# Kernel tuning notes

Hardware: AMD Instinct MI355X
Metric: run time of the kernel (lower is better)

Reference implementation:

```python
import jax, jax.numpy as jnp
import numpy as np


def _norm_group(pts, ref):
    # pts: [B,T,N,2], ref: [B,T,1,2]. Subtract reference point, divide both coords
    # by max(width,height) of the relative bbox (per frame), guarding scale==0.
    rel = pts - ref
    w = rel[..., 0].max(axis=-1) - rel[..., 0].min(axis=-1)
    h = rel[..., 1].max(axis=-1) - rel[..., 1].min(axis=-1)
    s = jnp.maximum(w, h)
    s = jnp.where(s == 0, jnp.ones_like(s), s)
    return rel / s[..., None, None]


def _prepare_input(x):
    B, T, _ = x.shape
    pts = x.reshape(B, T, 133, 2)
    left = _norm_group(pts[:, :, 91:112], pts[:, :, 9:10]).reshape(B, T, 42)
    right = _norm_group(pts[:, :, 112:133], pts[:, :, 10:11]).reshape(B, T, 42)
    center = pts[:, :, 0:1]
    left_arm = _norm_group(pts[:, :, (5, 7, 9), :], center).reshape(B, T, 6)
    right_arm = _norm_group(pts[:, :, (6, 8, 10), :], center).reshape(B, T, 6)
    return right, right_arm, left, left_arm


def _lstm(x, wih, whh, bih, bhh):
    # x: [B,T,F]; PyTorch gate order i,f,g,o. Returns all hidden states [B,T,H].
    B = x.shape[0]
    H = whh.shape[1]
    pre = jnp.einsum('btf,gf->btg', x, wih) + bih  # [B,T,4H]
    pre = pre.transpose(1, 0, 2)  # time-major for scan
    h0 = jnp.zeros((B, H), x.dtype)
    c0 = jnp.zeros((B, H), x.dtype)

    def step(carry, xt):
        h, c = carry
        g = xt + h @ whh.T + bhh
        i, f, gg, o = jnp.split(g, 4, axis=-1)
        i = jax.nn.sigmoid(i)
        f = jax.nn.sigmoid(f)
        gg = jnp.tanh(gg)
        o = jax.nn.sigmoid(o)
        c = f * c + i * gg
        h = o * jnp.tanh(c)
        return (h, c), h

    _, hs = jax.lax.scan(step, (h0, c0), pre)
    return hs.transpose(1, 0, 2)


def setup_inputs() -> dict:
    key = jax.random.key(0)
    ks = jax.random.split(key, 24)
    B, T = 128, 512
    NUM_CLASSES = 250
    HID = 2 * 64 + 2 * 32  # 192
    s = 0.1

    def p(k, shape):
        return jax.random.normal(k, shape, dtype=jnp.float32) * s

    inp = {'x': jax.random.normal(ks[0], (B, T, 266), dtype=jnp.float32)}
    # right hand LSTM: 42 -> 64
    inp['wih_rh'] = p(ks[1], (256, 42)); inp['whh_rh'] = p(ks[2], (256, 64))
    inp['bih_rh'] = p(ks[3], (256,));   inp['bhh_rh'] = p(ks[4], (256,))
    # right arm LSTM: 6 -> 32
    inp['wih_ra'] = p(ks[5], (128, 6));  inp['whh_ra'] = p(ks[6], (128, 32))
    inp['bih_ra'] = p(ks[7], (128,));   inp['bhh_ra'] = p(ks[8], (128,))
    # left hand LSTM: 42 -> 64
    inp['wih_lh'] = p(ks[9], (256, 42)); inp['whh_lh'] = p(ks[10], (256, 64))
    inp['bih_lh'] = p(ks[11], (256,));  inp['bhh_lh'] = p(ks[12], (256,))
    # left arm LSTM: 6 -> 32
    inp['wih_la'] = p(ks[13], (128, 6)); inp['whh_la'] = p(ks[14], (128, 32))
    inp['bih_la'] = p(ks[15], (128,));  inp['bhh_la'] = p(ks[16], (128,))
    # attention (Linear(192,1,bias=False)) and fc
    inp['att_w'] = p(ks[17], (1, HID))
    inp['fc_w'] = p(ks[18], (NUM_CLASSES, HID))
    inp['fc_b'] = p(ks[19], (NUM_CLASSES,))
    return inp


def reference(x, wih_rh, whh_rh, bih_rh, bhh_rh,
              wih_ra, whh_ra, bih_ra, bhh_ra,
              wih_lh, whh_lh, bih_lh, bhh_lh,
              wih_la, whh_la, bih_la, bhh_la,
              att_w, fc_w, fc_b):
    rh, ra, lh, la = _prepare_input(x)
    rh_out = _lstm(rh, wih_rh, whh_rh, bih_rh, bhh_rh)
    ra_out = _lstm(ra, wih_ra, whh_ra, bih_ra, bhh_ra)
    lh_out = _lstm(lh, wih_lh, whh_lh, bih_lh, bhh_lh)
    la_out = _lstm(la, wih_la, whh_la, bih_la, bhh_la)
    combined = jnp.concatenate([rh_out, ra_out, lh_out, la_out], axis=2)  # [B,T,192]
    scores = jnp.einsum('bth,oh->bto', combined, att_w)  # [B,T,1]
    weights = jax.nn.softmax(scores, axis=1)
    context = jnp.sum(weights * combined, axis=1)  # [B,192]
    out = context @ fc_w.T + fc_b  # [B,num_classes]
    return out, weights
```

## Files before the change

kernel.cpp:

```cpp
#include <hip/hip_runtime.h>
#include <math.h>

#define BATCH 128
#define TLEN 512
#define XF 266
#define HID 192
#define NC 250

typedef __attribute__((ext_vector_type(8))) short short8;
typedef __attribute__((ext_vector_type(4))) float float4v;

#define NL2E  -1.4426950408889634f
#define NL2E2 -2.8853900817779268f

__device__ __forceinline__ unsigned short f2bf(float f) {
  unsigned u = __float_as_uint(f);
  u += 0x7FFF + ((u >> 16) & 1);
  return (unsigned short)(u >> 16);
}
__device__ __forceinline__ float bf2f(unsigned short s) {
  return __uint_as_float(((unsigned)s) << 16);
}

__device__ __forceinline__ float exp2i(float x) {
#if __has_builtin(__builtin_amdgcn_exp2f)
  return __builtin_amdgcn_exp2f(x);
#else
  float r;
  asm("v_exp_f32 %0, %1" : "=v"(r) : "v"(x));
  return r;
#endif
}

__device__ __forceinline__ void lds_barrier() {
  asm volatile("s_waitcnt lgkmcnt(0)\n\ts_barrier" ::: "memory");
}


__device__ __forceinline__ void norm_hand(const float* __restrict__ xp,
                                          unsigned short* __restrict__ fp,
                                          int p0, int refp, int hs) {
  float rx = xp[2 * refp], ry = xp[2 * refp + 1];
  float px[21], py[21];
  float minx = 1e30f, maxx = -1e30f, miny = 1e30f, maxy = -1e30f;
#pragma unroll
  for (int i = 0; i < 21; ++i) {
    float ax = xp[2 * (p0 + i)] - rx;
    float ay = xp[2 * (p0 + i) + 1] - ry;
    px[i] = ax; py[i] = ay;
    minx = fminf(minx, ax); maxx = fmaxf(maxx, ax);
    miny = fminf(miny, ay); maxy = fmaxf(maxy, ay);
  }
  float s = fmaxf(maxx - minx, maxy - miny);
  if (s == 0.f) s = 1.f;
  float inv = 1.f / s;
#pragma unroll
  for (int i = 0; i < 21; ++i) {
    fp[2 * i] = f2bf(px[i] * inv);
    fp[2 * i + 1] = f2bf(py[i] * inv);
  }
  for (int i = 42; i < hs; ++i) fp[i] = 0;
}

__device__ __forceinline__ void norm_arm(const float* __restrict__ xp,
                                         unsigned short* __restrict__ fp,
                                         int a, int b, int c) {
  float rx = xp[0], ry = xp[1];
  float x0 = xp[2 * a] - rx, y0 = xp[2 * a + 1] - ry;
  float x1 = xp[2 * b] - rx, y1 = xp[2 * b + 1] - ry;
  float x2 = xp[2 * c] - rx, y2 = xp[2 * c + 1] - ry;
  float w = fmaxf(fmaxf(x0, x1), x2) - fminf(fminf(x0, x1), x2);
  float h = fmaxf(fmaxf(y0, y1), y2) - fminf(fminf(y0, y1), y2);
  float s = fmaxf(w, h);
  if (s == 0.f) s = 1.f;
  float inv = 1.f / s;
  fp[0] = f2bf(x0 * inv); fp[1] = f2bf(y0 * inv);
  fp[2] = f2bf(x1 * inv); fp[3] = f2bf(y1 * inv);
  fp[4] = f2bf(x2 * inv); fp[5] = f2bf(y2 * inv);
  fp[6] = 0; fp[7] = 0;
}

__global__ __launch_bounds__(256) void prep_kernel(
    const float* __restrict__ x,
    unsigned short* __restrict__ fHR, unsigned short* __restrict__ fHL,
    unsigned short* __restrict__ fAR, unsigned short* __restrict__ fAL,
    int mode) {
  int idx = blockIdx.x * 256 + threadIdx.x;
  if (idx >= BATCH * TLEN) return;
  int b = idx >> 9, t = idx & 511;
  const float* xp = x + (size_t)idx * XF;
  size_t hoff, aoff;
  int hs;
  if (mode) {
    hs = 64;
    int vh = b & 7;
    int rowh = (vh >> 1) * 4 + (vh & 1);
    hoff = (((size_t)(b >> 3) * TLEN + t) * 16 + rowh) * 64;
    int va = b & 15;
    int rowa = (va >> 3) * 16 + ((va & 7) >> 1) * 4 + (va & 1);
    aoff = (((size_t)(b >> 4) * TLEN + t) * 32 + rowa) * 8;
  } else {
    hs = 48;
    hoff = (((size_t)(b >> 4) * TLEN + t) * 16 + (b & 15)) * 48;
    aoff = (((size_t)(b >> 5) * TLEN + t) * 32 + (b & 31)) * 8;
  }
  norm_hand(xp, fHR + hoff, 112, 10, hs);
  norm_hand(xp, fHL + hoff, 91, 9, hs);
  norm_arm (xp, fAR + aoff, 6, 8, 10);
  norm_arm (xp, fAL + aoff, 5, 7, 9);
}


__global__ __launch_bounds__(256) void pack_kernel(
    int mode,
    const float* __restrict__ wi_rh, const float* __restrict__ wh_rh,
    const float* __restrict__ wi_ra, const float* __restrict__ wh_ra,
    const float* __restrict__ wi_lh, const float* __restrict__ wh_lh,
    const float* __restrict__ wi_la, const float* __restrict__ wh_la,
    unsigned short* __restrict__ btA_r, unsigned short* __restrict__ btA_l,
    unsigned short* __restrict__ btH_r, unsigned short* __restrict__ btH_l,
    unsigned short* __restrict__ btArm_r, unsigned short* __restrict__ btArm_l) {
  int blk = blockIdx.x, tid = threadIdx.x;
  if (blk < 2) {
    const float* wi = blk ? wi_lh : wi_rh;
    const float* wh = blk ? wh_lh : wh_rh;
    unsigned short* dst = blk ? btA_l : btA_r;
    if (mode) {
      for (int i = tid; i < 256 * 64; i += 256) {
        int g = i >> 6, k = i & 63;
        float s = ((g >> 6) == 2) ? NL2E2 : NL2E;
        dst[i] = f2bf(k < 42 ? wi[g * 42 + k] * s : 0.f);
      }
    } else {
      for (int i = tid; i < 256 * 128; i += 256) {
        int g = i >> 7, k = i & 127;
        float s = ((g >> 6) == 2) ? NL2E2 : NL2E;
        float v = (k < 42) ? wi[g * 42 + k] : (k < 64 ? 0.f : wh[g * 64 + (k - 64)]);
        dst[i] = f2bf(v * s);
      }
    }
  } else if (blk < 4) {
    if (mode) {
      const float* wh = (blk == 3) ? wh_lh : wh_rh;
      unsigned short* dst = (blk == 3) ? btH_l : btH_r;
      for (int i = tid; i < 256 * 64; i += 256) {
        int g = i >> 6;
        float s = ((g >> 6) == 2) ? NL2E2 : NL2E;
        dst[i] = f2bf(wh[i] * s);
      }
    }
  } else {
    const float* wi = (blk == 5) ? wi_la : wi_ra;
    const float* wh = (blk == 5) ? wh_la : wh_ra;
    unsigned short* dst = (blk == 5) ? btArm_l : btArm_r;
    for (int i = tid; i < 128 * 64; i += 256) {
      int g = i >> 6, k = i & 63;
      float s = ((g >> 5) == 2) ? NL2E2 : NL2E;
      float v = (k < 6) ? wi[g * 6 + k] : (k < 32 ? 0.f : wh[g * 32 + (k - 32)]);
      dst[i] = f2bf(v * s);
    }
  }
}


__global__ __launch_bounds__(256, 1) void pregemm_kernel(
    const unsigned short* __restrict__ f64R, const unsigned short* __restrict__ f64L,
    const unsigned short* __restrict__ btiR, const unsigned short* __restrict__ btiL,
    const float* __restrict__ biR, const float* __restrict__ bhR,
    const float* __restrict__ biL, const float* __restrict__ bhL,
    unsigned short* __restrict__ preR, unsigned short* __restrict__ preL) {
  int bx = blockIdx.x;
  int lr = bx >> 8, tile = (bx >> 4) & 15, tc = bx & 15;
  const unsigned short* f64 = lr ? f64L : f64R;
  const unsigned short* bti = lr ? btiL : btiR;
  const float* bi = lr ? biL : biR;
  const float* bh = lr ? bhL : bhR;
  unsigned short* pre = lr ? preL : preR;
  int tid = threadIdx.x, lane = tid & 63;
  int q = tid >> 6, n = lane & 15, quad = lane >> 4;
  float sq = (q == 2) ? NL2E2 : NL2E;

  short8 Vb[4][2];
  float bias[4];
#pragma unroll
  for (int jg = 0; jg < 4; ++jg) {
    int g = q * 64 + jg * 16 + n;
    bias[jg] = (bi[g] + bh[g]) * sq;
#pragma unroll
    for (int c = 0; c < 2; ++c)
      Vb[jg][c] = *(const short8*)(bti + (size_t)g * 64 + c * 32 + quad * 8);
  }

  for (int i = 0; i < 32; ++i) {
    int t = tc * 32 + i;
    const unsigned short* ap = f64 + ((size_t)(tile * 512 + t) * 16 + n) * 64 + quad * 8;
    short8 Va0 = *(const short8*)ap;
    short8 Va1 = *(const short8*)(ap + 32);
    unsigned short* pb = pre + (size_t)(tile * 512 + t) * 2048 + n * 32 + quad * 8 + q * 2;
#pragma unroll
    for (int jg = 0; jg < 4; ++jg) {
      float4v acc = {bias[jg], bias[jg], bias[jg], bias[jg]};
      acc = __builtin_amdgcn_mfma_f32_16x16x32_bf16(Va0, Vb[jg][0], acc, 0, 0, 0);
      acc = __builtin_amdgcn_mfma_f32_16x16x32_bf16(Va1, Vb[jg][1], acc, 0, 0, 0);
      unsigned w = (unsigned)f2bf(acc[0]) | ((unsigned)f2bf(acc[1]) << 16);
      *(unsigned*)(pb + (size_t)jg * 512) = w;
    }
  }
}


template <int H, int CH, int STR, int MB, int SCH, int HOFF, bool HOIST, int RV>
__device__ __forceinline__ void lstm_core(
    unsigned short* __restrict__ Ab0, unsigned short* __restrict__ Ab1,
    const unsigned short* __restrict__ Bt,
    const float* __restrict__ bi, const float* __restrict__ bh,
    const unsigned short* __restrict__ featp,
    const unsigned short* __restrict__ prep_,
    unsigned short* __restrict__ combbase,
    int b0, int mrow0, int j0) {
  constexpr int K = CH * 32;
  constexpr int XSH = MB * SCH * 8;
  constexpr int JQ = H / 4;
  constexpr int VR = (RV == 4) ? MB : MB / 2;
  int tid = threadIdx.x;
  int lane = tid & 63, n = lane & 15, quad = lane >> 4;

  short8 Vb[4][CH];
  float bias[4];
#pragma unroll
  for (int q = 0; q < 4; ++q) {
    int g = q * H + j0 + n;
    if (!HOIST) bias[q] = (bi[g] + bh[g]) * ((q == 2) ? NL2E2 : NL2E);
#pragma unroll
    for (int c = 0; c < CH; ++c)
      Vb[q][c] = *(const short8*)(Bt + (size_t)g * K + c * 32 + quad * 8);
  }

  for (int i = tid; i < MB * STR; i += 256) { Ab0[i] = 0; Ab1[i] = 0; }
  __syncthreads();

  bool st = false;
  unsigned short *xd0 = nullptr, *xd1 = nullptr;
  const unsigned short* fp = nullptr;
  short8 xE, xO;
  if (!HOIST) {
    st = tid < MB * SCH;
    int sm = tid / SCH, sc8 = tid % SCH;
    xd0 = Ab0 + sm * STR + sc8 * 8;
    xd1 = Ab1 + sm * STR + sc8 * 8;
    fp = featp + tid * 8;
    if (st) {
      *(short8*)xd0 = *(const short8*)fp;
      xO = *(const short8*)(fp + XSH);
      xE = *(const short8*)(fp + 2 * (size_t)XSH);
    }
    fp += 3 * (size_t)XSH;
  }

  const unsigned short* ppE = nullptr;
  const unsigned short* ppO = nullptr;
  short8 pE, pO;
  if (HOIST) {
    const unsigned short* pp0 = prep_ + (size_t)j0 * 32 + n * 32 + quad * 8;
    pE = *(const short8*)pp0;
    pO = *(const short8*)(pp0 + 2048);
    ppE = pp0 + 2 * (size_t)2048;
    ppO = pp0 + 3 * (size_t)2048;
  }

  float4v cc = {0.f, 0.f, 0.f, 0.f};
  __syncthreads();

  const unsigned short* ard0 = Ab0 + (mrow0 + n) * STR;
  const unsigned short* ard1 = Ab1 + (mrow0 + n) * STR;
  unsigned short* hw0 = Ab0 + (mrow0 + quad * 4) * STR + HOFF + j0 + n;
  unsigned short* hw1 = Ab1 + (mrow0 + quad * 4) * STR + HOFF + j0 + n;

  int vi = tid / JQ, fjq = tid % JQ;
  bool fon = tid < VR * JQ;
  int fm = (RV == 4) ? vi
                     : ((vi >> 3) * 16 + ((vi & 7) >> 1) * 4 + (vi & 1));
  const unsigned short* fl0 = Ab0 + fm * STR + HOFF + fjq * 4;
  const unsigned short* fl1 = Ab1 + fm * STR + HOFF + fjq * 4;
  unsigned short* cfp = combbase + ((size_t)(b0 + vi) * TLEN) * HID + fjq * 4;

#define ACT_AND_WRITE(hw)                                                     \
  _Pragma("unroll")                                                           \
  for (int r = 0; r < RV; ++r) {                                              \
    float Ei = exp2i(acc[0][r]);                                              \
    float Ef = exp2i(acc[1][r]);                                              \
    float Eg = exp2i(acc[2][r]);                                              \
    float Eo = exp2i(acc[3][r]);                                              \
    float gf = __builtin_amdgcn_rcpf(1.f + Ef);                               \
    float ig = (1.f - Eg) * __builtin_amdgcn_rcpf((1.f + Ei) * (1.f + Eg));   \
    float cv = fmaf(gf, cc[r], ig);                                           \
    cc[r] = cv;                                                               \
    float Ec = exp2i(cv * NL2E2);                                             \
    float hv = (1.f - Ec) * __builtin_amdgcn_rcpf((1.f + Eo) * (1.f + Ec));   \
    (hw)[r * STR] = f2bf(hv);                                                 \
  }

  for (int tt = 0; tt < TLEN; tt += 2) {
    {
      const int t = tt;
      if (fon && t > 0) {
        *(uint2*)cfp = *(const uint2*)fl0;
        cfp += HID;
      }
      short8 Va[CH];
#pragma unroll
      for (int c = 0; c < CH; ++c)
        Va[c] = *(const short8*)(ard0 + c * 32 + quad * 8);

      float4v acc[4];
      if (HOIST) {
#pragma unroll
        for (int q = 0; q < 4; ++q) {
          acc[q][0] = bf2f((unsigned short)pE[q * 2]);
          acc[q][1] = bf2f((unsigned short)pE[q * 2 + 1]);
          acc[q][2] = 0.f; acc[q][3] = 0.f;
        }
        if (t + 2 < TLEN) pE = *(const short8*)ppE;
        ppE += 2 * (size_t)2048;
      } else {
#pragma unroll
        for (int q = 0; q < 4; ++q)
          acc[q] = (float4v){bias[q], bias[q], bias[q], bias[q]};
      }
#pragma unroll
      for (int q = 0; q < 4; ++q)
#pragma unroll
        for (int c = 0; c < CH; ++c)
          acc[q] = __builtin_amdgcn_mfma_f32_16x16x32_bf16(Va[c], Vb[q][c], acc[q], 0, 0, 0);

      if (!HOIST) {
        if (st) {
          *(short8*)xd1 = xO;
          if (t + 3 < TLEN) xO = *(const short8*)fp;
        }
        fp += XSH;
      }

      ACT_AND_WRITE(hw1)
      lds_barrier();
    }
    {
      const int t = tt + 1;
      if (fon) {
        *(uint2*)cfp = *(const uint2*)fl1;
        cfp += HID;
      }
      short8 Va[CH];
#pragma unroll
      for (int c = 0; c < CH; ++c)
        Va[c] = *(const short8*)(ard1 + c * 32 + quad * 8);

      float4v acc[4];
      if (HOIST) {
#pragma unroll
        for (int q = 0; q < 4; ++q) {
          acc[q][0] = bf2f((unsigned short)pO[q * 2]);
          acc[q][1] = bf2f((unsigned short)pO[q * 2 + 1]);
          acc[q][2] = 0.f; acc[q][3] = 0.f;
        }
        if (t + 2 < TLEN) pO = *(const short8*)ppO;
        ppO += 2 * (size_t)2048;
      } else {
#pragma unroll
        for (int q = 0; q < 4; ++q)
          acc[q] = (float4v){bias[q], bias[q], bias[q], bias[q]};
      }
#pragma unroll
      for (int q = 0; q < 4; ++q)
#pragma unroll
        for (int c = 0; c < CH; ++c)
          acc[q] = __builtin_amdgcn_mfma_f32_16x16x32_bf16(Va[c], Vb[q][c], acc[q], 0, 0, 0);

      if (!HOIST) {
        if (st) {
          if (t + 1 < TLEN) *(short8*)xd0 = xE;
          if (t + 3 < TLEN) xE = *(const short8*)fp;
        }
        fp += XSH;
      }

      ACT_AND_WRITE(hw0)
      lds_barrier();
    }
  }

  if (fon) *(uint2*)cfp = *(const uint2*)fl0;
#undef ACT_AND_WRITE
}

__global__ __launch_bounds__(256, 1) void lstm_hoist(
    const unsigned short* __restrict__ fAR, const unsigned short* __restrict__ fAL,
    const unsigned short* __restrict__ btH_r, const unsigned short* __restrict__ btH_l,
    const unsigned short* __restrict__ btArm_r, const unsigned short* __restrict__ btArm_l,
    const unsigned short* __restrict__ preR, const unsigned short* __restrict__ preL,
    const float* __restrict__ b1i, const float* __restrict__ b1h,
    const float* __restrict__ b3i, const float* __restrict__ b3h,
    unsigned short* __restrict__ combined) {
  __shared__ __align__(16) unsigned short A0[2304];
  __shared__ __align__(16) unsigned short A1[2304];
  int blk = blockIdx.x;
  int wave = threadIdx.x >> 6;
  if (blk < 32) {
    int lr = blk >> 4, tl = blk & 15;
    lstm_core<64, 2, 72, 16, 0, 0, true, 2>(
        A0, A1, lr ? btH_l : btH_r, nullptr, nullptr, nullptr,
        (lr ? preL : preR) + (size_t)tl * 512 * 2048,
        combined + (lr ? 96 : 0), tl * 8, 0, wave * 16);
  } else {
    int a = blk - 32;
    int la = a >> 3, tl = a & 7;
    lstm_core<32, 2, 72, 32, 1, 32, false, 2>(
        A0, A1, la ? btArm_l : btArm_r, la ? b3i : b1i, la ? b3h : b1h,
        (la ? fAL : fAR) + (size_t)tl * 512 * 256, nullptr,
        combined + (la ? 160 : 64), tl * 16, (wave >> 1) * 16, (wave & 1) * 16);
  }
}

__global__ __launch_bounds__(256, 1) void lstm_fb(
    const unsigned short* __restrict__ fHR, const unsigned short* __restrict__ fHL,
    const unsigned short* __restrict__ fAR, const unsigned short* __restrict__ fAL,
    const unsigned short* __restrict__ btA_r, const unsigned short* __restrict__ btA_l,
    const unsigned short* __restrict__ btArm_r, const unsigned short* __restrict__ btArm_l,
    const float* __restrict__ b0i, const float* __restrict__ b0h,
    const float* __restrict__ b1i, const float* __restrict__ b1h,
    const float* __restrict__ b2i, const float* __restrict__ b2h,
    const float* __restrict__ b3i, const float* __restrict__ b3h,
    unsigned short* __restrict__ combined) {
  __shared__ __align__(16) unsigned short A0[2304];
  __shared__ __align__(16) unsigned short A1[2304];
  int blk = blockIdx.x;
  int wave = threadIdx.x >> 6;
  if (blk < 16) {
    int lr = blk >> 3, tl = blk & 7;
    lstm_core<64, 4, 136, 16, 6, 64, false, 4>(
        A0, A1, lr ? btA_l : btA_r, lr ? b2i : b0i, lr ? b2h : b0h,
        (lr ? fHL : fHR) + (size_t)tl * 512 * 768, nullptr,
        combined + (lr ? 96 : 0), tl * 16, 0, wave * 16);
  } else {
    int a = blk - 16;
    int la = a >> 2, tl = a & 3;
    lstm_core<32, 2, 72, 32, 1, 32, false, 4>(
        A0, A1, la ? btArm_l : btArm_r, la ? b3i : b1i, la ? b3h : b1h,
        (la ? fAL : fAR) + (size_t)tl * 512 * 256, nullptr,
        combined + (la ? 160 : 64), tl * 32, (wave >> 1) * 16, (wave & 1) * 16);
  }
}


__global__ __launch_bounds__(512) void attn_kernel(const unsigned short* __restrict__ combined,
                                                   const float* __restrict__ att_w,
                                                   const float* __restrict__ fc_w,
                                                   const float* __restrict__ fc_b,
                                                   float* __restrict__ dout) {
  __shared__ float sc[TLEN];
  __shared__ float aw[HID];
  __shared__ float pctx[8][HID];
  __shared__ float ctx[HID];
  __shared__ float red[8];
  int b = blockIdx.x, tid = threadIdx.x;
  int lane = tid & 63, wave = tid >> 6;
  const unsigned short* cb = combined + (size_t)b * TLEN * HID;
  if (tid < HID) aw[tid] = att_w[tid];
  __syncthreads();
  float a0 = aw[lane], a1 = aw[lane + 64], a2 = aw[lane + 128];

  int t0 = wave * 64;
  for (int t = t0; t < t0 + 64; t += 2) {
    const unsigned short* r0 = cb + (size_t)t * HID;
    const unsigned short* r1 = r0 + HID;
    float p0 = a0 * bf2f(r0[lane]) + a1 * bf2f(r0[lane + 64]) + a2 * bf2f(r0[lane + 128]);
    float p1 = a0 * bf2f(r1[lane]) + a1 * bf2f(r1[lane + 64]) + a2 * bf2f(r1[lane + 128]);
#pragma unroll
    for (int o = 32; o; o >>= 1) {
      p0 += __shfl_xor(p0, o, 64);
      p1 += __shfl_xor(p1, o, 64);
    }
    if (lane == 0) { sc[t] = p0; sc[t + 1] = p1; }
  }
  __syncthreads();

  float e = sc[tid];
  float lmax = e;
#pragma unroll
  for (int o = 32; o; o >>= 1) lmax = fmaxf(lmax, __shfl_xor(lmax, o, 64));
  if (lane == 0) red[wave] = lmax;
  __syncthreads();
  float m = red[0];
#pragma unroll
  for (int w = 1; w < 8; ++w) m = fmaxf(m, red[w]);
  __syncthreads();
  float ex = __expf(e - m);
  float ls = ex;
#pragma unroll
  for (int o = 32; o; o >>= 1) ls += __shfl_xor(ls, o, 64);
  if (lane == 0) red[wave] = ls;
  __syncthreads();
  float S = red[0];
#pragma unroll
  for (int w = 1; w < 8; ++w) S += red[w];
  float wgt = ex / S;
  sc[tid] = wgt;
  dout[BATCH * NC + b * TLEN + tid] = wgt;
  __syncthreads();

#pragma unroll
  for (int p = 0; p < 3; ++p) {
    int h = p * 64 + lane;
    float c0 = 0.f, c1 = 0.f, c2 = 0.f, c3 = 0.f;
    for (int t = t0; t < t0 + 64; t += 4) {
      c0 += sc[t] * bf2f(cb[(size_t)t * HID + h]);
      c1 += sc[t + 1] * bf2f(cb[(size_t)(t + 1) * HID + h]);
      c2 += sc[t + 2] * bf2f(cb[(size_t)(t + 2) * HID + h]);
      c3 += sc[t + 3] * bf2f(cb[(size_t)(t + 3) * HID + h]);
    }
    pctx[wave][h] = (c0 + c1) + (c2 + c3);
  }
  __syncthreads();
  if (tid < HID) {
    float s = pctx[0][tid];
#pragma unroll
    for (int w = 1; w < 8; ++w) s += pctx[w][tid];
    ctx[tid] = s;
  }
  __syncthreads();

  if (tid < NC) {
    const float* wr = fc_w + (size_t)tid * HID;
    float s0 = fc_b[tid], s1 = 0.f, s2 = 0.f, s3 = 0.f;
#pragma unroll
    for (int h = 0; h < HID; h += 4) {
      s0 += ctx[h] * wr[h];
      s1 += ctx[h + 1] * wr[h + 1];
      s2 += ctx[h + 2] * wr[h + 2];
      s3 += ctx[h + 3] * wr[h + 3];
    }
    dout[b * NC + tid] = (s0 + s1) + (s2 + s3);
  }
}


extern "C" void kernel_launch(void* const* d_in, const int* in_sizes, int n_in,
                              void* d_out, int out_size, void* d_ws, size_t ws_size,
                              hipStream_t stream) {
  const float* x = (const float*)d_in[0];
  const float* wih_rh = (const float*)d_in[1];
  const float* whh_rh = (const float*)d_in[2];
  const float* bih_rh = (const float*)d_in[3];
  const float* bhh_rh = (const float*)d_in[4];
  const float* wih_ra = (const float*)d_in[5];
  const float* whh_ra = (const float*)d_in[6];
  const float* bih_ra = (const float*)d_in[7];
  const float* bhh_ra = (const float*)d_in[8];
  const float* wih_lh = (const float*)d_in[9];
  const float* whh_lh = (const float*)d_in[10];
  const float* bih_lh = (const float*)d_in[11];
  const float* bhh_lh = (const float*)d_in[12];
  const float* wih_la = (const float*)d_in[13];
  const float* whh_la = (const float*)d_in[14];
  const float* bih_la = (const float*)d_in[15];
  const float* bhh_la = (const float*)d_in[16];
  const float* att_w = (const float*)d_in[17];
  const float* fc_w = (const float*)d_in[18];
  const float* fc_b = (const float*)d_in[19];

  const size_t SZ_COMB   = (size_t)BATCH * TLEN * HID * 2;
  const size_t SZ_FARM_H = (size_t)8 * TLEN * 32 * 8 * 2;
  const size_t SZ_FARM_F = (size_t)4 * TLEN * 32 * 8 * 2;
  const size_t SZ_F64    = (size_t)16 * TLEN * 16 * 64 * 2;
  const size_t SZ_F48    = (size_t)8 * TLEN * 16 * 48 * 2;
  const size_t SZ_PRE    = (size_t)16 * TLEN * 2048 * 2;
  const size_t NEED_FULL = SZ_COMB + 2 * SZ_FARM_H + 2 * SZ_F64 + 2 * SZ_PRE +
                           2 * 32768 + 2 * 32768 + 2 * 16384;
  bool hoist = ws_size >= NEED_FULL;

  char* p = (char*)d_ws;
  unsigned short* combined = (unsigned short*)p; p += SZ_COMB;
  unsigned short *fAR, *fAL;
  unsigned short *fHR, *fHL, *preR = nullptr, *preL = nullptr;
  unsigned short *btA_r, *btA_l, *btH_r = nullptr, *btH_l = nullptr, *btArm_r, *btArm_l;
  if (hoist) {
    fAR = (unsigned short*)p; p += SZ_FARM_H;
    fAL = (unsigned short*)p; p += SZ_FARM_H;
    fHR = (unsigned short*)p; p += SZ_F64;
    fHL = (unsigned short*)p; p += SZ_F64;
    preR = (unsigned short*)p; p += SZ_PRE;
    preL = (unsigned short*)p; p += SZ_PRE;
    btA_r = (unsigned short*)p; p += 32768;
    btA_l = (unsigned short*)p; p += 32768;
    btH_r = (unsigned short*)p; p += 32768;
    btH_l = (unsigned short*)p; p += 32768;
  } else {
    fAR = (unsigned short*)p; p += SZ_FARM_F;
    fAL = (unsigned short*)p; p += SZ_FARM_F;
    fHR = (unsigned short*)p; p += SZ_F48;
    fHL = (unsigned short*)p; p += SZ_F48;
    btA_r = (unsigned short*)p; p += 65536;
    btA_l = (unsigned short*)p; p += 65536;
    btH_r = btA_r; btH_l = btA_l;
  }
  btArm_r = (unsigned short*)p; p += 16384;
  btArm_l = (unsigned short*)p;

  prep_kernel<<<dim3((BATCH * TLEN + 255) / 256), 256, 0, stream>>>(
      x, fHR, fHL, fAR, fAL, hoist ? 1 : 0);
  pack_kernel<<<dim3(6), 256, 0, stream>>>(
      hoist ? 1 : 0,
      wih_rh, whh_rh, wih_ra, whh_ra, wih_lh, whh_lh, wih_la, whh_la,
      btA_r, btA_l, btH_r, btH_l, btArm_r, btArm_l);
  if (hoist) {
    pregemm_kernel<<<dim3(512), 256, 0, stream>>>(
        fHR, fHL, btA_r, btA_l, bih_rh, bhh_rh, bih_lh, bhh_lh, preR, preL);
    lstm_hoist<<<dim3(48), 256, 0, stream>>>(
        fAR, fAL, btH_r, btH_l, btArm_r, btArm_l, preR, preL,
        bih_ra, bhh_ra, bih_la, bhh_la, combined);
  } else {
    lstm_fb<<<dim3(24), 256, 0, stream>>>(
        fHR, fHL, fAR, fAL, btA_r, btA_l, btArm_r, btArm_l,
        bih_rh, bhh_rh, bih_ra, bhh_ra, bih_lh, bhh_lh, bih_la, bhh_la, combined);
  }
  attn_kernel<<<dim3(BATCH), 512, 0, stream>>>(combined, att_w, fc_w, fc_b, (float*)d_out);
}
```

Before: 438.8 us.

## Split hoisted LSTM rows across twice the blocks and fuse weight packing

The hoisted LSTM path now launches 96 blocks instead of 48. Each block handles a single MFMA accumulator row (RSEL) per batch pair, which shortens the per-step activation work on the serial recurrence critical path. The pre-activation buffer is re-laid out so each block reads only its row's gates with a compact uint2 load. The weight pack kernel is removed from the hoisted path, and pregemm and the LSTM kernels convert fp32 weights to bf16 inline. The cost is doubled MFMA work per useful output, since three of the four rows are wasted, and more blocks competing for the GPU.

```diff
diff --git a/kernel.cpp b/kernel.cpp
--- a/kernel.cpp
+++ b/kernel.cpp
@@ -112,47 +112,27 @@
 
 
 __global__ __launch_bounds__(256) void pack_kernel(
-    int mode,
     const float* __restrict__ wi_rh, const float* __restrict__ wh_rh,
     const float* __restrict__ wi_ra, const float* __restrict__ wh_ra,
     const float* __restrict__ wi_lh, const float* __restrict__ wh_lh,
     const float* __restrict__ wi_la, const float* __restrict__ wh_la,
     unsigned short* __restrict__ btA_r, unsigned short* __restrict__ btA_l,
-    unsigned short* __restrict__ btH_r, unsigned short* __restrict__ btH_l,
     unsigned short* __restrict__ btArm_r, unsigned short* __restrict__ btArm_l) {
   int blk = blockIdx.x, tid = threadIdx.x;
   if (blk < 2) {
     const float* wi = blk ? wi_lh : wi_rh;
     const float* wh = blk ? wh_lh : wh_rh;
     unsigned short* dst = blk ? btA_l : btA_r;
-    if (mode) {
-      for (int i = tid; i < 256 * 64; i += 256) {
-        int g = i >> 6, k = i & 63;
-        float s = ((g >> 6) == 2) ? NL2E2 : NL2E;
-        dst[i] = f2bf(k < 42 ? wi[g * 42 + k] * s : 0.f);
-      }
-    } else {
-      for (int i = tid; i < 256 * 128; i += 256) {
-        int g = i >> 7, k = i & 127;
-        float s = ((g >> 6) == 2) ? NL2E2 : NL2E;
-        float v = (k < 42) ? wi[g * 42 + k] : (k < 64 ? 0.f : wh[g * 64 + (k - 64)]);
-        dst[i] = f2bf(v * s);
-      }
-    }
-  } else if (blk < 4) {
-    if (mode) {
-      const float* wh = (blk == 3) ? wh_lh : wh_rh;
-      unsigned short* dst = (blk == 3) ? btH_l : btH_r;
-      for (int i = tid; i < 256 * 64; i += 256) {
-        int g = i >> 6;
-        float s = ((g >> 6) == 2) ? NL2E2 : NL2E;
-        dst[i] = f2bf(wh[i] * s);
-      }
+    for (int i = tid; i < 256 * 128; i += 256) {
+      int g = i >> 7, k = i & 127;
+      float s = ((g >> 6) == 2) ? NL2E2 : NL2E;
+      float v = (k < 42) ? wi[g * 42 + k] : (k < 64 ? 0.f : wh[g * 64 + (k - 64)]);
+      dst[i] = f2bf(v * s);
     }
   } else {
-    const float* wi = (blk == 5) ? wi_la : wi_ra;
-    const float* wh = (blk == 5) ? wh_la : wh_ra;
-    unsigned short* dst = (blk == 5) ? btArm_l : btArm_r;
+    const float* wi = (blk == 3) ? wi_la : wi_ra;
+    const float* wh = (blk == 3) ? wh_la : wh_ra;
+    unsigned short* dst = (blk == 3) ? btArm_l : btArm_r;
     for (int i = tid; i < 128 * 64; i += 256) {
       int g = i >> 6, k = i & 63;
       float s = ((g >> 5) == 2) ? NL2E2 : NL2E;
@@ -165,14 +145,14 @@
 
 __global__ __launch_bounds__(256, 1) void pregemm_kernel(
     const unsigned short* __restrict__ f64R, const unsigned short* __restrict__ f64L,
-    const unsigned short* __restrict__ btiR, const unsigned short* __restrict__ btiL,
+    const float* __restrict__ wiR, const float* __restrict__ wiL,
     const float* __restrict__ biR, const float* __restrict__ bhR,
     const float* __restrict__ biL, const float* __restrict__ bhL,
     unsigned short* __restrict__ preR, unsigned short* __restrict__ preL) {
   int bx = blockIdx.x;
   int lr = bx >> 8, tile = (bx >> 4) & 15, tc = bx & 15;
   const unsigned short* f64 = lr ? f64L : f64R;
-  const unsigned short* bti = lr ? btiL : btiR;
+  const float* wi = lr ? wiL : wiR;
   const float* bi = lr ? biL : biR;
   const float* bh = lr ? bhL : bhR;
   unsigned short* pre = lr ? preL : preR;
@@ -187,8 +167,15 @@
     int g = q * 64 + jg * 16 + n;
     bias[jg] = (bi[g] + bh[g]) * sq;
 #pragma unroll
-    for (int c = 0; c < 2; ++c)
-      Vb[jg][c] = *(const short8*)(bti + (size_t)g * 64 + c * 32 + quad * 8);
+    for (int c = 0; c < 2; ++c) {
+      short8 vb;
+#pragma unroll
+      for (int s = 0; s < 8; ++s) {
+        int k = c * 32 + quad * 8 + s;
+        vb[s] = (short)f2bf(k < 42 ? wi[g * 42 + k] * sq : 0.f);
+      }
+      Vb[jg][c] = vb;
+    }
   }
 
   for (int i = 0; i < 32; ++i) {
@@ -196,32 +183,31 @@
     const unsigned short* ap = f64 + ((size_t)(tile * 512 + t) * 16 + n) * 64 + quad * 8;
     short8 Va0 = *(const short8*)ap;
     short8 Va1 = *(const short8*)(ap + 32);
-    unsigned short* pb = pre + (size_t)(tile * 512 + t) * 2048 + n * 32 + quad * 8 + q * 2;
+    unsigned short* pb0 = pre + ((size_t)(tile * 2) * 512 + t) * 1024 + n * 16 + quad * 4 + q;
+    unsigned short* pb1 = pb0 + (size_t)512 * 1024;
 #pragma unroll
     for (int jg = 0; jg < 4; ++jg) {
       float4v acc = {bias[jg], bias[jg], bias[jg], bias[jg]};
       acc = __builtin_amdgcn_mfma_f32_16x16x32_bf16(Va0, Vb[jg][0], acc, 0, 0, 0);
       acc = __builtin_amdgcn_mfma_f32_16x16x32_bf16(Va1, Vb[jg][1], acc, 0, 0, 0);
-      unsigned w = (unsigned)f2bf(acc[0]) | ((unsigned)f2bf(acc[1]) << 16);
-      *(unsigned*)(pb + (size_t)jg * 512) = w;
-    }
-  }
-}
-
-
-template <int H, int CH, int STR, int MB, int SCH, int HOFF, bool HOIST, int RV>
-__device__ __forceinline__ void lstm_core(
+      pb0[jg * 256] = f2bf(acc[0]);
+      pb1[jg * 256] = f2bf(acc[1]);
+    }
+  }
+}
+
+
+template <int H, int CH, int STR, int MB, int SCH, int HOFF, bool HOIST, int RSEL>
+__device__ __forceinline__ void lstm_core1(
     unsigned short* __restrict__ Ab0, unsigned short* __restrict__ Ab1,
-    const unsigned short* __restrict__ Bt,
+    const float* __restrict__ wq,
+    const float* __restrict__ wx,
     const float* __restrict__ bi, const float* __restrict__ bh,
     const unsigned short* __restrict__ featp,
     const unsigned short* __restrict__ prep_,
     unsigned short* __restrict__ combbase,
     int b0, int mrow0, int j0) {
-  constexpr int K = CH * 32;
   constexpr int XSH = MB * SCH * 8;
-  constexpr int JQ = H / 4;
-  constexpr int VR = (RV == 4) ? MB : MB / 2;
   int tid = threadIdx.x;
   int lane = tid & 63, n = lane & 15, quad = lane >> 4;
 
@@ -229,11 +215,26 @@
   float bias[4];
 #pragma unroll
   for (int q = 0; q < 4; ++q) {
+    float sq = (q == 2) ? NL2E2 : NL2E;
     int g = q * H + j0 + n;
-    if (!HOIST) bias[q] = (bi[g] + bh[g]) * ((q == 2) ? NL2E2 : NL2E);
-#pragma unroll
-    for (int c = 0; c < CH; ++c)
-      Vb[q][c] = *(const short8*)(Bt + (size_t)g * K + c * 32 + quad * 8);
+    if (!HOIST) bias[q] = (bi[g] + bh[g]) * sq;
+#pragma unroll
+    for (int c = 0; c < CH; ++c) {
+      short8 vb;
+#pragma unroll
+      for (int s = 0; s < 8; ++s) {
+        int k = c * 32 + quad * 8 + s;
+        float v;
+        if (HOIST) {
+          v = wq[(size_t)g * H + k];
+        } else {
+          v = (k < 6) ? wx[g * 6 + k]
+                      : (k >= 32 ? wq[g * 32 + (k - 32)] : 0.f);
+        }
+        vb[s] = (short)f2bf(v * sq);
+      }
+      Vb[q][c] = vb;
+    }
   }
 
   for (int i = tid; i < MB * STR; i += 256) { Ab0[i] = 0; Ab1[i] = 0; }
@@ -245,9 +246,8 @@
   short8 xE, xO;
   if (!HOIST) {
     st = tid < MB * SCH;
-    int sm = tid / SCH, sc8 = tid % SCH;
-    xd0 = Ab0 + sm * STR + sc8 * 8;
-    xd1 = Ab1 + sm * STR + sc8 * 8;
+    xd0 = Ab0 + tid * STR;
+    xd1 = Ab1 + tid * STR;
     fp = featp + tid * 8;
     if (st) {
       *(short8*)xd0 = *(const short8*)fp;
@@ -257,16 +257,221 @@
     fp += 3 * (size_t)XSH;
   }
 
-  const unsigned short* ppE = nullptr;
-  const unsigned short* ppO = nullptr;
-  short8 pE, pO;
+  const unsigned short *ppE = nullptr, *ppO = nullptr;
+  uint2 pE = {0, 0}, pO = {0, 0};
   if (HOIST) {
-    const unsigned short* pp0 = prep_ + (size_t)j0 * 32 + n * 32 + quad * 8;
-    pE = *(const short8*)pp0;
-    pO = *(const short8*)(pp0 + 2048);
-    ppE = pp0 + 2 * (size_t)2048;
-    ppO = pp0 + 3 * (size_t)2048;
-  }
+    const unsigned short* pp0 = prep_ + (size_t)(j0 >> 4) * 256 + n * 16 + quad * 4;
+    pE = *(const uint2*)pp0;
+    pO = *(const uint2*)(pp0 + 1024);
+    ppE = pp0 + 2 * 1024;
+    ppO = pp0 + 3 * 1024;
+  }
+
+  float cc = 0.f;
+  __syncthreads();
+
+  const unsigned short* ard0 = Ab0 + (mrow0 + n) * STR;
+  const unsigned short* ard1 = Ab1 + (mrow0 + n) * STR;
+  unsigned short* hw0 = Ab0 + (mrow0 + quad * 4 + RSEL) * STR + HOFF + j0 + n;
+  unsigned short* hw1 = Ab1 + (mrow0 + quad * 4 + RSEL) * STR + HOFF + j0 + n;
+  unsigned short* cgp = combbase +
+      ((size_t)(b0 + (mrow0 >> 1) + quad * 2) * TLEN) * HID + j0 + n;
+
+  for (int tt = 0; tt < TLEN; tt += 2) {
+    {
+      const int t = tt;
+      short8 Va[CH];
+#pragma unroll
+      for (int c = 0; c < CH; ++c)
+        Va[c] = *(const short8*)(ard0 + c * 32 + quad * 8);
+
+      float4v acc[4];
+#pragma unroll
+      for (int q = 0; q < 4; ++q) acc[q] = (float4v){0.f, 0.f, 0.f, 0.f};
+      if (HOIST) {
+        acc[0][RSEL] = __uint_as_float(pE.x << 16);
+        acc[1][RSEL] = __uint_as_float(pE.x & 0xffff0000u);
+        acc[2][RSEL] = __uint_as_float(pE.y << 16);
+        acc[3][RSEL] = __uint_as_float(pE.y & 0xffff0000u);
+        if (t + 2 < TLEN) pE = *(const uint2*)ppE;
+        ppE += 2 * 1024;
+      } else {
+#pragma unroll
+        for (int q = 0; q < 4; ++q) acc[q][RSEL] = bias[q];
+      }
+#pragma unroll
+      for (int q = 0; q < 4; ++q)
+#pragma unroll
+        for (int c = 0; c < CH; ++c)
+          acc[q] = __builtin_amdgcn_mfma_f32_16x16x32_bf16(Va[c], Vb[q][c], acc[q], 0, 0, 0);
+
+      if (!HOIST) {
+        if (st) {
+          *(short8*)xd1 = xO;
+          if (t + 3 < TLEN) xO = *(const short8*)fp;
+        }
+        fp += XSH;
+      }
+
+      float Ei = exp2i(acc[0][RSEL]);
+      float Ef = exp2i(acc[1][RSEL]);
+      float Eg = exp2i(acc[2][RSEL]);
+      float Eo = exp2i(acc[3][RSEL]);
+      float gf = __builtin_amdgcn_rcpf(1.f + Ef);
+      float ig = (1.f - Eg) * __builtin_amdgcn_rcpf((1.f + Ei) * (1.f + Eg));
+      float cv = fmaf(gf, cc, ig);
+      cc = cv;
+      float Ec = exp2i(cv * NL2E2);
+      float hv = (1.f - Ec) * __builtin_amdgcn_rcpf((1.f + Eo) * (1.f + Ec));
+      unsigned short hb = f2bf(hv);
+      hw1[0] = hb;
+      *cgp = hb;
+      cgp += HID;
+      lds_barrier();
+    }
+    {
+      const int t = tt + 1;
+      short8 Va[CH];
+#pragma unroll
+      for (int c = 0; c < CH; ++c)
+        Va[c] = *(const short8*)(ard1 + c * 32 + quad * 8);
+
+      float4v acc[4];
+#pragma unroll
+      for (int q = 0; q < 4; ++q) acc[q] = (float4v){0.f, 0.f, 0.f, 0.f};
+      if (HOIST) {
+        acc[0][RSEL] = __uint_as_float(pO.x << 16);
+        acc[1][RSEL] = __uint_as_float(pO.x & 0xffff0000u);
+        acc[2][RSEL] = __uint_as_float(pO.y << 16);
+        acc[3][RSEL] = __uint_as_float(pO.y & 0xffff0000u);
+        if (t + 2 < TLEN) pO = *(const uint2*)ppO;
+        ppO += 2 * 1024;
+      } else {
+#pragma unroll
+        for (int q = 0; q < 4; ++q) acc[q][RSEL] = bias[q];
+      }
+#pragma unroll
+      for (int q = 0; q < 4; ++q)
+#pragma unroll
+        for (int c = 0; c < CH; ++c)
+          acc[q] = __builtin_amdgcn_mfma_f32_16x16x32_bf16(Va[c], Vb[q][c], acc[q], 0, 0, 0);
+
+      if (!HOIST) {
+        if (st) {
+          if (t + 1 < TLEN) *(short8*)xd0 = xE;
+          if (t + 3 < TLEN) xE = *(const short8*)fp;
+        }
+        fp += XSH;
+      }
+
+      float Ei = exp2i(acc[0][RSEL]);
+      float Ef = exp2i(acc[1][RSEL]);
+      float Eg = exp2i(acc[2][RSEL]);
+      float Eo = exp2i(acc[3][RSEL]);
+      float gf = __builtin_amdgcn_rcpf(1.f + Ef);
+      float ig = (1.f - Eg) * __builtin_amdgcn_rcpf((1.f + Ei) * (1.f + Eg));
+      float cv = fmaf(gf, cc, ig);
+      cc = cv;
+      float Ec = exp2i(cv * NL2E2);
+      float hv = (1.f - Ec) * __builtin_amdgcn_rcpf((1.f + Eo) * (1.f + Ec));
+      unsigned short hb = f2bf(hv);
+      hw0[0] = hb;
+      *cgp = hb;
+      cgp += HID;
+      lds_barrier();
+    }
+  }
+}
+
+__global__ __launch_bounds__(256, 1) void lstm_hoist(
+    const unsigned short* __restrict__ fAR, const unsigned short* __restrict__ fAL,
+    const float* __restrict__ whh_rh, const float* __restrict__ whh_lh,
+    const float* __restrict__ wih_ra, const float* __restrict__ whh_ra,
+    const float* __restrict__ wih_la, const float* __restrict__ whh_la,
+    const unsigned short* __restrict__ preR, const unsigned short* __restrict__ preL,
+    const float* __restrict__ b1i, const float* __restrict__ b1h,
+    const float* __restrict__ b3i, const float* __restrict__ b3h,
+    unsigned short* __restrict__ combined) {
+  __shared__ __align__(16) unsigned short A0[2304];
+  __shared__ __align__(16) unsigned short A1[2304];
+  int blk = blockIdx.x;
+  int wave = threadIdx.x >> 6;
+  if (blk < 64) {
+    int lr = blk >> 5, rem = blk & 31, tl = rem >> 1, r = rem & 1;
+    const unsigned short* pp = (lr ? preL : preR) + (size_t)rem * 512 * 1024;
+    const float* wq = lr ? whh_lh : whh_rh;
+    unsigned short* cmb = combined + (lr ? 96 : 0);
+    if (r == 0)
+      lstm_core1<64, 2, 72, 16, 0, 0, true, 0>(
+          A0, A1, wq, nullptr, nullptr, nullptr, nullptr, pp, cmb,
+          tl * 8 + 0, 0, wave * 16);
+    else
+      lstm_core1<64, 2, 72, 16, 0, 0, true, 1>(
+          A0, A1, wq, nullptr, nullptr, nullptr, nullptr, pp, cmb,
+          tl * 8 + 1, 0, wave * 16);
+  } else {
+    int a = blk - 64;
+    int la = a >> 4, rem = a & 15, tl = rem >> 1, r = rem & 1;
+    const unsigned short* fpz = (la ? fAL : fAR) + (size_t)tl * 512 * 256;
+    const float* wxp = la ? wih_la : wih_ra;
+    const float* wqp = la ? whh_la : whh_ra;
+    const float* bip = la ? b3i : b1i;
+    const float* bhp = la ? b3h : b1h;
+    unsigned short* cmb = combined + (la ? 160 : 64);
+    int mrow0 = (wave >> 1) * 16, j0 = (wave & 1) * 16;
+    if (r == 0)
+      lstm_core1<32, 2, 72, 32, 1, 32, false, 0>(
+          A0, A1, wqp, wxp, bip, bhp, fpz, nullptr, cmb,
+          tl * 16 + 0, mrow0, j0);
+    else
+      lstm_core1<32, 2, 72, 32, 1, 32, false, 1>(
+          A0, A1, wqp, wxp, bip, bhp, fpz, nullptr, cmb,
+          tl * 16 + 1, mrow0, j0);
+  }
+}
+
+
+template <int H, int CH, int STR, int MB, int SCH, int HOFF, int RV>
+__device__ __forceinline__ void lstm_core_fb(
+    unsigned short* __restrict__ Ab0, unsigned short* __restrict__ Ab1,
+    const unsigned short* __restrict__ Bt,
+    const float* __restrict__ bi, const float* __restrict__ bh,
+    const unsigned short* __restrict__ featp,
+    unsigned short* __restrict__ combbase,
+    int b0, int mrow0, int j0) {
+  constexpr int K = CH * 32;
+  constexpr int XSH = MB * SCH * 8;
+  constexpr int JQ = H / 4;
+  constexpr int VR = MB;
+  int tid = threadIdx.x;
+  int lane = tid & 63, n = lane & 15, quad = lane >> 4;
+
+  short8 Vb[4][CH];
+  float bias[4];
+#pragma unroll
+  for (int q = 0; q < 4; ++q) {
+    int g = q * H + j0 + n;
+    bias[q] = (bi[g] + bh[g]) * ((q == 2) ? NL2E2 : NL2E);
+#pragma unroll
+    for (int c = 0; c < CH; ++c)
+      Vb[q][c] = *(const short8*)(Bt + (size_t)g * K + c * 32 + quad * 8);
+  }
+
+  for (int i = tid; i < MB * STR; i += 256) { Ab0[i] = 0; Ab1[i] = 0; }
+  __syncthreads();
+
+  bool st = tid < MB * SCH;
+  int sm = SCH ? tid / SCH : 0, sc8 = SCH ? tid % SCH : 0;
+  unsigned short* xd0 = Ab0 + sm * STR + sc8 * 8;
+  unsigned short* xd1 = Ab1 + sm * STR + sc8 * 8;
+  const unsigned short* fp = featp + tid * 8;
+  short8 xE, xO;
+  if (st) {
+    *(short8*)xd0 = *(const short8*)fp;
+    xO = *(const short8*)(fp + XSH);
+    xE = *(const short8*)(fp + 2 * (size_t)XSH);
+  }
+  fp += 3 * (size_t)XSH;
 
   float4v cc = {0.f, 0.f, 0.f, 0.f};
   __syncthreads();
@@ -278,13 +483,12 @@
 
   int vi = tid / JQ, fjq = tid % JQ;
   bool fon = tid < VR * JQ;
-  int fm = (RV == 4) ? vi
-                     : ((vi >> 3) * 16 + ((vi & 7) >> 1) * 4 + (vi & 1));
+  int fm = vi;
   const unsigned short* fl0 = Ab0 + fm * STR + HOFF + fjq * 4;
   const unsigned short* fl1 = Ab1 + fm * STR + HOFF + fjq * 4;
   unsigned short* cfp = combbase + ((size_t)(b0 + vi) * TLEN) * HID + fjq * 4;
 
-#define ACT_AND_WRITE(hw)                                                     \
+#define ACT_FB(hw)                                                            \
   _Pragma("unroll")                                                           \
   for (int r = 0; r < RV; ++r) {                                              \
     float Ei = exp2i(acc[0][r]);                                              \
@@ -311,37 +515,21 @@
 #pragma unroll
       for (int c = 0; c < CH; ++c)
         Va[c] = *(const short8*)(ard0 + c * 32 + quad * 8);
-
       float4v acc[4];
-      if (HOIST) {
-#pragma unroll
-        for (int q = 0; q < 4; ++q) {
-          acc[q][0] = bf2f((unsigned short)pE[q * 2]);
-          acc[q][1] = bf2f((unsigned short)pE[q * 2 + 1]);
-          acc[q][2] = 0.f; acc[q][3] = 0.f;
-        }
-        if (t + 2 < TLEN) pE = *(const short8*)ppE;
-        ppE += 2 * (size_t)2048;
-      } else {
-#pragma unroll
-        for (int q = 0; q < 4; ++q)
-          acc[q] = (float4v){bias[q], bias[q], bias[q], bias[q]};
-      }
+#pragma unroll
+      for (int q = 0; q < 4; ++q)
+        acc[q] = (float4v){bias[q], bias[q], bias[q], bias[q]};
 #pragma unroll
       for (int q = 0; q < 4; ++q)
 #pragma unroll
         for (int c = 0; c < CH; ++c)
           acc[q] = __builtin_amdgcn_mfma_f32_16x16x32_bf16(Va[c], Vb[q][c], acc[q], 0, 0, 0);
-
-      if (!HOIST) {
-        if (st) {
-          *(short8*)xd1 = xO;
-          if (t + 3 < TLEN) xO = *(const short8*)fp;
-        }
-        fp += XSH;
-      }
-
-      ACT_AND_WRITE(hw1)
+      if (st) {
+        *(short8*)xd1 = xO;
+        if (t + 3 < TLEN) xO = *(const short8*)fp;
+      }
+      fp += XSH;
+      ACT_FB(hw1)
       lds_barrier();
     }
     {
@@ -354,71 +542,26 @@
 #pragma unroll
       for (int c = 0; c < CH; ++c)
         Va[c] = *(const short8*)(ard1 + c * 32 + quad * 8);
-
       float4v acc[4];
-      if (HOIST) {
-#pragma unroll
-        for (int q = 0; q < 4; ++q) {
-          acc[q][0] = bf2f((unsigned short)pO[q * 2]);
-          acc[q][1] = bf2f((unsigned short)pO[q * 2 + 1]);
-          acc[q][2] = 0.f; acc[q][3] = 0.f;
-        }
-        if (t + 2 < TLEN) pO = *(const short8*)ppO;
-        ppO += 2 * (size_t)2048;
-      } else {
-#pragma unroll
-        for (int q = 0; q < 4; ++q)
-          acc[q] = (float4v){bias[q], bias[q], bias[q], bias[q]};
-      }
+#pragma unroll
+      for (int q = 0; q < 4; ++q)
+        acc[q] = (float4v){bias[q], bias[q], bias[q], bias[q]};
 #pragma unroll
       for (int q = 0; q < 4; ++q)
 #pragma unroll
         for (int c = 0; c < CH; ++c)
           acc[q] = __builtin_amdgcn_mfma_f32_16x16x32_bf16(Va[c], Vb[q][c], acc[q], 0, 0, 0);
-
-      if (!HOIST) {
-        if (st) {
-          if (t + 1 < TLEN) *(short8*)xd0 = xE;
-          if (t + 3 < TLEN) xE = *(const short8*)fp;
-        }
-        fp += XSH;
-      }
-
-      ACT_AND_WRITE(hw0)
+      if (st) {
+        if (t + 1 < TLEN) *(short8*)xd0 = xE;
+        if (t + 3 < TLEN) xE = *(const short8*)fp;
+      }
+      fp += XSH;
+      ACT_FB(hw0)
       lds_barrier();
     }
   }
-
   if (fon) *(uint2*)cfp = *(const uint2*)fl0;
-#undef ACT_AND_WRITE
-}
-
-__global__ __launch_bounds__(256, 1) void lstm_hoist(
-    const unsigned short* __restrict__ fAR, const unsigned short* __restrict__ fAL,
-    const unsigned short* __restrict__ btH_r, const unsigned short* __restrict__ btH_l,
-    const unsigned short* __restrict__ btArm_r, const unsigned short* __restrict__ btArm_l,
-    const unsigned short* __restrict__ preR, const unsigned short* __restrict__ preL,
-    const float* __restrict__ b1i, const float* __restrict__ b1h,
-    const float* __restrict__ b3i, const float* __restrict__ b3h,
-    unsigned short* __restrict__ combined) {
-  __shared__ __align__(16) unsigned short A0[2304];
-  __shared__ __align__(16) unsigned short A1[2304];
-  int blk = blockIdx.x;
-  int wave = threadIdx.x >> 6;
-  if (blk < 32) {
-    int lr = blk >> 4, tl = blk & 15;
-    lstm_core<64, 2, 72, 16, 0, 0, true, 2>(
-        A0, A1, lr ? btH_l : btH_r, nullptr, nullptr, nullptr,
-        (lr ? preL : preR) + (size_t)tl * 512 * 2048,
-        combined + (lr ? 96 : 0), tl * 8, 0, wave * 16);
-  } else {
-    int a = blk - 32;
-    int la = a >> 3, tl = a & 7;
-    lstm_core<32, 2, 72, 32, 1, 32, false, 2>(
-        A0, A1, la ? btArm_l : btArm_r, la ? b3i : b1i, la ? b3h : b1h,
-        (la ? fAL : fAR) + (size_t)tl * 512 * 256, nullptr,
-        combined + (la ? 160 : 64), tl * 16, (wave >> 1) * 16, (wave & 1) * 16);
-  }
+#undef ACT_FB
 }
 
 __global__ __launch_bounds__(256, 1) void lstm_fb(
@@ -437,16 +580,16 @@
   int wave = threadIdx.x >> 6;
   if (blk < 16) {
     int lr = blk >> 3, tl = blk & 7;
-    lstm_core<64, 4, 136, 16, 6, 64, false, 4>(
+    lstm_core_fb<64, 4, 136, 16, 6, 64, 4>(
         A0, A1, lr ? btA_l : btA_r, lr ? b2i : b0i, lr ? b2h : b0h,
-        (lr ? fHL : fHR) + (size_t)tl * 512 * 768, nullptr,
+        (lr ? fHL : fHR) + (size_t)tl * 512 * 768,
         combined + (lr ? 96 : 0), tl * 16, 0, wave * 16);
   } else {
     int a = blk - 16;
     int la = a >> 2, tl = a & 3;
-    lstm_core<32, 2, 72, 32, 1, 32, false, 4>(
+    lstm_core_fb<32, 2, 72, 32, 1, 32, 4>(
         A0, A1, la ? btArm_l : btArm_r, la ? b3i : b1i, la ? b3h : b1h,
-        (la ? fAL : fAR) + (size_t)tl * 512 * 256, nullptr,
+        (la ? fAL : fAR) + (size_t)tl * 512 * 256,
         combined + (la ? 160 : 64), tl * 32, (wave >> 1) * 16, (wave & 1) * 16);
   }
 }
@@ -573,16 +716,15 @@
   const size_t SZ_FARM_F = (size_t)4 * TLEN * 32 * 8 * 2;
   const size_t SZ_F64    = (size_t)16 * TLEN * 16 * 64 * 2;
   const size_t SZ_F48    = (size_t)8 * TLEN * 16 * 48 * 2;
-  const size_t SZ_PRE    = (size_t)16 * TLEN * 2048 * 2;
-  const size_t NEED_FULL = SZ_COMB + 2 * SZ_FARM_H + 2 * SZ_F64 + 2 * SZ_PRE +
-                           2 * 32768 + 2 * 32768 + 2 * 16384;
+  const size_t SZ_PRE    = (size_t)32 * TLEN * 1024 * 2;
+  const size_t NEED_FULL = SZ_COMB + 2 * SZ_FARM_H + 2 * SZ_F64 + 2 * SZ_PRE;
   bool hoist = ws_size >= NEED_FULL;
 
   char* p = (char*)d_ws;
   unsigned short* combined = (unsigned short*)p; p += SZ_COMB;
   unsigned short *fAR, *fAL;
   unsigned short *fHR, *fHL, *preR = nullptr, *preL = nullptr;
-  unsigned short *btA_r, *btA_l, *btH_r = nullptr, *btH_l = nullptr, *btArm_r, *btArm_l;
+  unsigned short *btA_r = nullptr, *btA_l = nullptr, *btArm_r = nullptr, *btArm_l = nullptr;
   if (hoist) {
     fAR = (unsigned short*)p; p += SZ_FARM_H;
     fAL = (unsigned short*)p; p += SZ_FARM_H;
@@ -590,10 +732,6 @@
     fHL = (unsigned short*)p; p += SZ_F64;
     preR = (unsigned short*)p; p += SZ_PRE;
     preL = (unsigned short*)p; p += SZ_PRE;
-    btA_r = (unsigned short*)p; p += 32768;
-    btA_l = (unsigned short*)p; p += 32768;
-    btH_r = (unsigned short*)p; p += 32768;
-    btH_l = (unsigned short*)p; p += 32768;
   } else {
     fAR = (unsigned short*)p; p += SZ_FARM_F;
     fAL = (unsigned short*)p; p += SZ_FARM_F;
@@ -601,24 +739,22 @@
     fHL = (unsigned short*)p; p += SZ_F48;
     btA_r = (unsigned short*)p; p += 65536;
     btA_l = (unsigned short*)p; p += 65536;
-    btH_r = btA_r; btH_l = btA_l;
-  }
-  btArm_r = (unsigned short*)p; p += 16384;
-  btArm_l = (unsigned short*)p;
+    btArm_r = (unsigned short*)p; p += 16384;
+    btArm_l = (unsigned short*)p;
+  }
 
   prep_kernel<<<dim3((BATCH * TLEN + 255) / 256), 256, 0, stream>>>(
       x, fHR, fHL, fAR, fAL, hoist ? 1 : 0);
-  pack_kernel<<<dim3(6), 256, 0, stream>>>(
-      hoist ? 1 : 0,
-      wih_rh, whh_rh, wih_ra, whh_ra, wih_lh, whh_lh, wih_la, whh_la,
-      btA_r, btA_l, btH_r, btH_l, btArm_r, btArm_l);
   if (hoist) {
     pregemm_kernel<<<dim3(512), 256, 0, stream>>>(
-        fHR, fHL, btA_r, btA_l, bih_rh, bhh_rh, bih_lh, bhh_lh, preR, preL);
-    lstm_hoist<<<dim3(48), 256, 0, stream>>>(
-        fAR, fAL, btH_r, btH_l, btArm_r, btArm_l, preR, preL,
-        bih_ra, bhh_ra, bih_la, bhh_la, combined);
+        fHR, fHL, wih_rh, wih_lh, bih_rh, bhh_rh, bih_lh, bhh_lh, preR, preL);
+    lstm_hoist<<<dim3(96), 256, 0, stream>>>(
+        fAR, fAL, whh_rh, whh_lh, wih_ra, whh_ra, wih_la, whh_la,
+        preR, preL, bih_ra, bhh_ra, bih_la, bhh_la, combined);
   } else {
+    pack_kernel<<<dim3(4), 256, 0, stream>>>(
+        wih_rh, whh_rh, wih_ra, whh_ra, wih_lh, whh_lh, wih_la, whh_la,
+        btA_r, btA_l, btArm_r, btArm_l);
     lstm_fb<<<dim3(24), 256, 0, stream>>>(
         fHR, fHL, fAR, fAL, btA_r, btA_l, btArm_r, btArm_l,
         bih_rh, bhh_rh, bih_ra, bhh_ra, bih_lh, bhh_lh, bih_la, bhh_la, combined);
```

Result: no change. 430.3 us (-1.9%).
